# Performance work log

Measured on AMD Instinct MI355X. Metric: run time of the kernel, lower is better.

## Reference

```python
import jax, jax.numpy as jnp
import numpy as np

N_NODES = 40000
N_EDGES = 640000
IN_DIM = 7
HID = 128
N_LAYERS = 5


def setup_inputs() -> dict:
    key = jax.random.key(0)
    ks = jax.random.split(key, 12)
    x = jax.random.normal(ks[0], (N_NODES, IN_DIM), dtype=jnp.float32)
    edge_index = jax.random.randint(ks[1], (2, N_EDGES), 0, N_NODES, dtype=jnp.int64)
    # shift distances away from 0 so 1/d^2 weights stay finite across 5 layers
    dist = jax.random.uniform(ks[2], (N_EDGES,), dtype=jnp.float32) + 0.5
    s_enc = 1.0 / np.sqrt(IN_DIM)
    s_hid = 1.0 / np.sqrt(HID)
    enc_W = jax.random.normal(ks[3], (HID, IN_DIM), dtype=jnp.float32) * s_enc
    enc_b = jax.random.normal(ks[4], (HID,), dtype=jnp.float32) * 0.01
    conv_W = jax.random.normal(ks[5], (N_LAYERS, HID, HID), dtype=jnp.float32) * s_hid * 0.2
    conv_b = jax.random.normal(ks[6], (N_LAYERS, HID), dtype=jnp.float32) * 0.01
    cluster_W = jax.random.normal(ks[7], (3, HID), dtype=jnp.float32) * s_hid
    cluster_b = jax.random.normal(ks[8], (3,), dtype=jnp.float32) * 0.01
    energy_W = jax.random.normal(ks[9], (1, HID), dtype=jnp.float32) * s_hid
    energy_b = jax.random.normal(ks[10], (1,), dtype=jnp.float32) * 0.01
    return {"x": x, "edge_index": edge_index, "dist": dist,
            "enc_W": enc_W, "enc_b": enc_b,
            "conv_W": conv_W, "conv_b": conv_b,
            "cluster_W": cluster_W, "cluster_b": cluster_b,
            "energy_W": energy_W, "energy_b": energy_b}


def reference(x, edge_index, dist, enc_W, enc_b, conv_W, conv_b,
              cluster_W, cluster_b, energy_W, energy_b):
    n = x.shape[0]
    src = edge_index[0]  # x_j: source nodes (PyG source_to_target flow)
    dst = edge_index[1]  # aggregation target
    w = 1.0 / jnp.square(dist + 1e-6)  # [E]
    h = x @ enc_W.T + enc_b  # [N, H]
    for l in range(conv_W.shape[0]):
        # gather -> linear -> inverse-square weight -> scatter-add
        msg = (h[src] @ conv_W[l].T + conv_b[l]) * w[:, None]  # [E, H]
        h = jax.nn.relu(jax.ops.segment_sum(msg, dst, num_segments=n))
    cluster_probs = jax.nn.softmax(h @ cluster_W.T + cluster_b, axis=-1)  # [N, 3]
    energy = h.mean(axis=0, keepdims=True) @ energy_W.T + energy_b  # [1, 1]
    stable = energy < -1.0
    return cluster_probs, energy, stable
```

## Files before the change

kernel.cpp:

```cpp
#include <hip/hip_runtime.h>
#include <hip/hip_fp16.h>

#define NN 40000
#define NE 640000
#define HID 128
#define NL 5
#define NBLK 157

typedef __attribute__((ext_vector_type(8))) short bf16x8;
typedef __attribute__((ext_vector_type(4))) float f32x4;

static __device__ __forceinline__ unsigned short f32_to_bf16_rne(float f) {
  unsigned int u = __float_as_uint(f);
  unsigned int lsb = (u >> 16) & 1u;
  u += 0x7fffu + lsb;
  return (unsigned short)(u >> 16);
}
static __device__ __forceinline__ float bf16_to_f32(unsigned short s) {
  return __uint_as_float(((unsigned int)s) << 16);
}

__global__ void encoder_wconv_kernel(const float* __restrict__ x, const float* __restrict__ encW,
                                     const float* __restrict__ encb, __half* __restrict__ h,
                                     const float* __restrict__ convW,
                                     unsigned short* __restrict__ whi,
                                     unsigned short* __restrict__ wlo) {
  int b = blockIdx.x;
  if (b < 20000) {
    int gid = b * 256 + threadIdx.x;
    int n = gid >> 7, k = gid & 127;
    const float* xp = x + n * 7;
    const float* wp = encW + k * 7;
    float acc = encb[k];
#pragma unroll
    for (int i = 0; i < 7; ++i) acc += xp[i] * wp[i];
    h[gid] = __float2half(acc);
  } else {
    int i = (b - 20000) * 256 + threadIdx.x;
    if (i < NL * HID * HID) {
      float w = convW[i];
      unsigned short hi = f32_to_bf16_rne(w);
      unsigned short lo = f32_to_bf16_rne(w - bf16_to_f32(hi));
      whi[i] = hi;
      wlo[i] = lo;
    }
  }
}

__global__ void hist_kernel(const int* __restrict__ dst, int* __restrict__ cnt,
                            int* __restrict__ rank) {
  int e = blockIdx.x * blockDim.x + threadIdx.x;
  if (e < NE) rank[e] = atomicAdd(&cnt[dst[e]], 1);
}

__global__ void partial_kernel(const int* __restrict__ cnt, int* __restrict__ blocksum) {
  __shared__ int red[4];
  int t = threadIdx.x;
  int idx = blockIdx.x * 256 + t;
  int v = idx < NN ? cnt[idx] : 0;
#pragma unroll
  for (int off = 32; off > 0; off >>= 1) v += __shfl_xor(v, off, 64);
  if ((t & 63) == 0) red[t >> 6] = v;
  __syncthreads();
  if (t == 0) blocksum[blockIdx.x] = red[0] + red[1] + red[2] + red[3];
}

__global__ void scan_small_kernel(const int* __restrict__ blocksum, int* __restrict__ blockoff,
                                  int* __restrict__ row_ptr) {
  __shared__ int sh[256];
  int t = threadIdx.x;
  int v = t < NBLK ? blocksum[t] : 0;
  sh[t] = v;
  __syncthreads();
  for (int off = 1; off < 256; off <<= 1) {
    int u = (t >= off) ? sh[t - off] : 0;
    __syncthreads();
    sh[t] += u;
    __syncthreads();
  }
  if (t < NBLK) blockoff[t] = sh[t] - v;
  if (t == 255) row_ptr[NN] = sh[255];
}

__global__ void rowptr_kernel(const int* __restrict__ cnt, const int* __restrict__ blockoff,
                              int* __restrict__ row_ptr) {
  __shared__ int sh[256];
  int t = threadIdx.x;
  int idx = blockIdx.x * 256 + t;
  int v = idx < NN ? cnt[idx] : 0;
  sh[t] = v;
  __syncthreads();
  for (int off = 1; off < 256; off <<= 1) {
    int u = (t >= off) ? sh[t - off] : 0;
    __syncthreads();
    sh[t] += u;
    __syncthreads();
  }
  if (idx < NN) row_ptr[idx] = blockoff[blockIdx.x] + sh[t] - v;
}

__global__ void scatter_kernel(const int* __restrict__ src, const int* __restrict__ dst,
                               const float* __restrict__ dist,
                               const int* __restrict__ row_ptr, const int* __restrict__ rank,
                               int2* __restrict__ csr_ew) {
  int e = blockIdx.x * blockDim.x + threadIdx.x;
  if (e >= NE) return;
  int pos = row_ptr[dst[e]] + rank[e];
  float dd = dist[e] + 1e-6f;
  float w = 1.0f / (dd * dd);
  csr_ew[pos] = make_int2(src[e], (int)__float_as_uint(w));
}

__global__ void wsum_kernel(const int* __restrict__ row_ptr, const int2* __restrict__ csr_ew,
                            float* __restrict__ wsum) {
  int n = blockIdx.x * blockDim.x + threadIdx.x;
  if (n >= NN) return;
  int s = row_ptr[n], e = row_ptr[n + 1];
  float acc = 0.f;
  for (int i = s; i < e; ++i) acc += __uint_as_float((unsigned)csr_ew[i].y);
  wsum[n] = acc;
}

__global__ void aggregate_kernel(const __half* __restrict__ h, const int* __restrict__ row_ptr,
                                 const int2* __restrict__ csr_ew,
                                 unsigned short* __restrict__ aggh,
                                 unsigned short* __restrict__ aggl) {
  int wid = (blockIdx.x * blockDim.x + threadIdx.x) >> 6;
  int lane = threadIdx.x & 63;
  if (wid >= NN) return;
  int s = __builtin_amdgcn_readfirstlane(row_ptr[wid]);
  int e = __builtin_amdgcn_readfirstlane(row_ptr[wid + 1]);
  int g = lane >> 4;
  int k = lane & 15;
  const __half* hp = h + k * 8;
  float a[8] = {0.f, 0.f, 0.f, 0.f, 0.f, 0.f, 0.f, 0.f};
  int i = s;
  for (; i + 16 <= e; i += 16) {
    uint4 hv[4];
    float wv[4];
#pragma unroll
    for (int u = 0; u < 4; ++u) {
      int2 p = csr_ew[i + u * 4 + g];
      wv[u] = __uint_as_float((unsigned)p.y);
      hv[u] = *reinterpret_cast<const uint4*>(hp + (size_t)p.x * HID);
    }
#pragma unroll
    for (int u = 0; u < 4; ++u) {
      const __half2* q = reinterpret_cast<const __half2*>(&hv[u]);
#pragma unroll
      for (int c = 0; c < 4; ++c) {
        float2 f = __half22float2(q[c]);
        a[2 * c] += wv[u] * f.x;
        a[2 * c + 1] += wv[u] * f.y;
      }
    }
  }
  for (; i < e; i += 4) {
    int j = i + g;
    int jc = j < e ? j : e - 1;
    int2 p = csr_ew[jc];
    float w = (j < e) ? __uint_as_float((unsigned)p.y) : 0.f;
    uint4 hv = *reinterpret_cast<const uint4*>(hp + (size_t)p.x * HID);
    const __half2* q = reinterpret_cast<const __half2*>(&hv);
#pragma unroll
    for (int c = 0; c < 4; ++c) {
      float2 f = __half22float2(q[c]);
      a[2 * c] += w * f.x;
      a[2 * c + 1] += w * f.y;
    }
  }
#pragma unroll
  for (int c = 0; c < 8; ++c) {
    a[c] += __shfl_xor(a[c], 16, 64);
    a[c] += __shfl_xor(a[c], 32, 64);
  }
  if (g == 0) {
    unsigned short hh[8], ll[8];
#pragma unroll
    for (int c = 0; c < 8; ++c) {
      hh[c] = f32_to_bf16_rne(a[c]);
      ll[c] = f32_to_bf16_rne(a[c] - bf16_to_f32(hh[c]));
    }
    *reinterpret_cast<uint4*>(aggh + wid * HID + k * 8) = *reinterpret_cast<const uint4*>(hh);
    *reinterpret_cast<uint4*>(aggl + wid * HID + k * 8) = *reinterpret_cast<const uint4*>(ll);
  }
}

__global__ void __launch_bounds__(256) mfma_linear_kernel(
    const unsigned short* __restrict__ aggh, const unsigned short* __restrict__ aggl,
    const unsigned short* __restrict__ whi, const unsigned short* __restrict__ wlo,
    const float* __restrict__ wsum, const float* __restrict__ b, __half* __restrict__ h) {
  int wave = threadIdx.x >> 6;
  int lane = threadIdx.x & 63;
  int node0 = blockIdx.x * 64 + wave * 16;
  int mrow = lane & 15;
  int kc = (lane >> 4) * 8;

  const unsigned short* pah = aggh + (node0 + mrow) * HID;
  const unsigned short* pal = aggl + (node0 + mrow) * HID;

  f32x4 acc[8];
#pragma unroll
  for (int t = 0; t < 8; ++t) acc[t] = (f32x4){0.f, 0.f, 0.f, 0.f};

#pragma unroll
  for (int s = 0; s < 4; ++s) {
    int joff = s * 32 + kc;
    bf16x8 ah = *reinterpret_cast<const bf16x8*>(pah + joff);
    bf16x8 al = *reinterpret_cast<const bf16x8*>(pal + joff);
#pragma unroll
    for (int t = 0; t < 8; ++t) {
      bf16x8 bh = *reinterpret_cast<const bf16x8*>(whi + (t * 16 + mrow) * HID + joff);
      bf16x8 bl = *reinterpret_cast<const bf16x8*>(wlo + (t * 16 + mrow) * HID + joff);
      acc[t] = __builtin_amdgcn_mfma_f32_16x16x32_bf16(ah, bh, acc[t], 0, 0, 0);
      acc[t] = __builtin_amdgcn_mfma_f32_16x16x32_bf16(ah, bl, acc[t], 0, 0, 0);
      acc[t] = __builtin_amdgcn_mfma_f32_16x16x32_bf16(al, bh, acc[t], 0, 0, 0);
    }
  }

  int nodeBase = node0 + (lane >> 4) * 4;
  float ws4[4];
#pragma unroll
  for (int r = 0; r < 4; ++r) ws4[r] = wsum[nodeBase + r];
#pragma unroll
  for (int t = 0; t < 8; ++t) {
    int kout = t * 16 + mrow;
    float bk = b[kout];
#pragma unroll
    for (int r = 0; r < 4; ++r) {
      float v = acc[t][r] + bk * ws4[r];
      h[(nodeBase + r) * HID + kout] = __float2half(fmaxf(v, 0.f));
    }
  }
}

__global__ void cluster_kernel(const __half* __restrict__ h, const float* __restrict__ cW,
                               const float* __restrict__ cb, float* __restrict__ out) {
  int wid = (blockIdx.x * blockDim.x + threadIdx.x) >> 6;
  int lane = threadIdx.x & 63;
  if (wid >= NN) return;
  float h0 = __half2float(h[wid * HID + lane]);
  float h1 = __half2float(h[wid * HID + 64 + lane]);
  float logit[3];
#pragma unroll
  for (int c = 0; c < 3; ++c) {
    float p = h0 * cW[c * HID + lane] + h1 * cW[c * HID + 64 + lane];
#pragma unroll
    for (int off = 32; off > 0; off >>= 1) p += __shfl_xor(p, off, 64);
    logit[c] = p + cb[c];
  }
  if (lane == 0) {
    float m = fmaxf(logit[0], fmaxf(logit[1], logit[2]));
    float e0 = expf(logit[0] - m), e1 = expf(logit[1] - m), e2 = expf(logit[2] - m);
    float inv = 1.0f / (e0 + e1 + e2);
    out[wid * 3 + 0] = e0 * inv;
    out[wid * 3 + 1] = e1 * inv;
    out[wid * 3 + 2] = e2 * inv;
  }
}

__global__ void colsum_part_kernel(const __half* __restrict__ h, float* __restrict__ partial) {
  int t = threadIdx.x;
  int col = t & 127;
  int lane_id = blockIdx.x * 2 + (t >> 7);
  float acc = 0.f;
  for (int r = lane_id; r < NN; r += 2048) acc += __half2float(h[r * HID + col]);
  partial[lane_id * HID + col] = acc;
}

__global__ void energy_final_kernel(const float* __restrict__ partial,
                                    const float* __restrict__ eW, const float* __restrict__ eb,
                                    float* __restrict__ out) {
  __shared__ float sh[8][HID];
  __shared__ float red[2];
  int t = threadIdx.x;
  int col = t & 127;
  int slot = t >> 7;
  float acc = 0.f;
  for (int i = 0; i < 256; ++i) acc += partial[(slot + 8 * i) * HID + col];
  sh[slot][col] = acc;
  __syncthreads();
  if (t < 128) {
    float s = 0.f;
#pragma unroll
    for (int j = 0; j < 8; ++j) s += sh[j][t];
    float v = s * (1.0f / NN) * eW[t];
#pragma unroll
    for (int off = 32; off > 0; off >>= 1) v += __shfl_xor(v, off, 64);
    if ((t & 63) == 0) red[t >> 6] = v;
  }
  __syncthreads();
  if (t == 0) {
    float e = red[0] + red[1] + eb[0];
    out[NN * 3] = e;
    out[NN * 3 + 1] = (e < -1.0f) ? 1.0f : 0.0f;
  }
}

extern "C" void kernel_launch(void* const* d_in, const int* in_sizes, int n_in,
                              void* d_out, int out_size, void* d_ws, size_t ws_size,
                              hipStream_t stream) {
  const float* x    = (const float*)d_in[0];
  const int*   ei   = (const int*)d_in[1];
  const float* dist = (const float*)d_in[2];
  const float* encW = (const float*)d_in[3];
  const float* encb = (const float*)d_in[4];
  const float* convW = (const float*)d_in[5];
  const float* convb = (const float*)d_in[6];
  const float* cW   = (const float*)d_in[7];
  const float* cb   = (const float*)d_in[8];
  const float* eW   = (const float*)d_in[9];
  const float* eb   = (const float*)d_in[10];
  float* out = (float*)d_out;

  char* ws = (char*)d_ws;
  __half*         h       = (__half*)        (ws + 0);
  unsigned short* aggh    = (unsigned short*)(ws + 10240000);
  unsigned short* aggl    = (unsigned short*)(ws + 20480000);
  int2*           csr_ew  = (int2*)          (ws + 30720000);
  int*            row_ptr = (int*)           (ws + 35840000);
  int*            cnt     = (int*)           (ws + 36000064);
  float*          wsum    = (float*)         (ws + 36160064);
  unsigned short* whi5    = (unsigned short*)(ws + 36320064);
  unsigned short* wlo5    = (unsigned short*)(ws + 36483904);
  int*            rank    = (int*)           (ws + 36647744);
  if (ws_size < (size_t)39207744) return;

  int*   blocksum = (int*)aggh;
  int*   blockoff = (int*)aggh + 512;
  float* partial  = (float*)aggh;

  const int* srcI = ei;
  const int* dstI = ei + NE;

  hipMemsetAsync(cnt, 0, 160000, stream);

  encoder_wconv_kernel<<<20320, 256, 0, stream>>>(x, encW, encb, h, convW, whi5, wlo5);

  hist_kernel<<<(NE + 255) / 256, 256, 0, stream>>>(dstI, cnt, rank);
  partial_kernel<<<NBLK, 256, 0, stream>>>(cnt, blocksum);
  scan_small_kernel<<<1, 256, 0, stream>>>(blocksum, blockoff, row_ptr);
  rowptr_kernel<<<NBLK, 256, 0, stream>>>(cnt, blockoff, row_ptr);
  scatter_kernel<<<(NE + 255) / 256, 256, 0, stream>>>(srcI, dstI, dist, row_ptr, rank, csr_ew);
  wsum_kernel<<<(NN + 255) / 256, 256, 0, stream>>>(row_ptr, csr_ew, wsum);

  for (int l = 0; l < NL; ++l) {
    aggregate_kernel<<<(NN * 64 + 255) / 256, 256, 0, stream>>>(h, row_ptr, csr_ew, aggh, aggl);
    mfma_linear_kernel<<<NN / 64, 256, 0, stream>>>(aggh, aggl,
                                                    whi5 + (size_t)l * HID * HID,
                                                    wlo5 + (size_t)l * HID * HID,
                                                    wsum, convb + (size_t)l * HID, h);
  }

  cluster_kernel<<<(NN * 64 + 255) / 256, 256, 0, stream>>>(h, cW, cb, out);
  colsum_part_kernel<<<1024, 256, 0, stream>>>(h, partial);
  energy_final_kernel<<<1, 1024, 0, stream>>>(partial, eW, eb, out);
}
```

Before: 381.6 us.

## Fuse neighbor aggregation and MFMA linear into one per-layer kernel via LDS

Merges the per-layer aggregate and MFMA linear kernels into one kernel. Each 1024-thread block aggregates 16 nodes (one wave per node) into LDS as bf16 hi/lo splits, then 8 waves each compute one 16-column output tile with MFMA. The hi/lo global round-trip and one launch per layer go away, and h is ping-ponged between two buffers to avoid read/write races. In exchange, half the waves sit idle during the MFMA phase, weights are reloaded per 16-node block, and the large blocks with a barrier may reduce latency hiding for the gather.

```diff
diff --git a/kernel.cpp b/kernel.cpp
--- a/kernel.cpp
+++ b/kernel.cpp
@@ -6,6 +6,7 @@
 #define HID 128
 #define NL 5
 #define NBLK 157
+#define LSTRIDE 136
 
 typedef __attribute__((ext_vector_type(8))) short bf16x8;
 typedef __attribute__((ext_vector_type(4))) float f32x4;
@@ -121,116 +122,103 @@
   wsum[n] = acc;
 }
 
-__global__ void aggregate_kernel(const __half* __restrict__ h, const int* __restrict__ row_ptr,
-                                 const int2* __restrict__ csr_ew,
-                                 unsigned short* __restrict__ aggh,
-                                 unsigned short* __restrict__ aggl) {
-  int wid = (blockIdx.x * blockDim.x + threadIdx.x) >> 6;
+__global__ void __launch_bounds__(1024) fused_layer_kernel(
+    const __half* __restrict__ hin, const int* __restrict__ row_ptr,
+    const int2* __restrict__ csr_ew,
+    const unsigned short* __restrict__ whi, const unsigned short* __restrict__ wlo,
+    const float* __restrict__ wsum, const float* __restrict__ b,
+    __half* __restrict__ hout) {
+  __shared__ __align__(16) unsigned short sAh[16][LSTRIDE];
+  __shared__ __align__(16) unsigned short sAl[16][LSTRIDE];
+  int wave = threadIdx.x >> 6;
   int lane = threadIdx.x & 63;
-  if (wid >= NN) return;
-  int s = __builtin_amdgcn_readfirstlane(row_ptr[wid]);
-  int e = __builtin_amdgcn_readfirstlane(row_ptr[wid + 1]);
-  int g = lane >> 4;
-  int k = lane & 15;
-  const __half* hp = h + k * 8;
-  float a[8] = {0.f, 0.f, 0.f, 0.f, 0.f, 0.f, 0.f, 0.f};
-  int i = s;
-  for (; i + 16 <= e; i += 16) {
-    uint4 hv[4];
-    float wv[4];
-#pragma unroll
-    for (int u = 0; u < 4; ++u) {
-      int2 p = csr_ew[i + u * 4 + g];
-      wv[u] = __uint_as_float((unsigned)p.y);
-      hv[u] = *reinterpret_cast<const uint4*>(hp + (size_t)p.x * HID);
-    }
-#pragma unroll
-    for (int u = 0; u < 4; ++u) {
-      const __half2* q = reinterpret_cast<const __half2*>(&hv[u]);
+  int wid = blockIdx.x * 16 + wave;
+
+  {
+    int s = __builtin_amdgcn_readfirstlane(row_ptr[wid]);
+    int e = __builtin_amdgcn_readfirstlane(row_ptr[wid + 1]);
+    int g = lane >> 4;
+    int k = lane & 15;
+    const __half* hp = hin + k * 8;
+    float a[8] = {0.f, 0.f, 0.f, 0.f, 0.f, 0.f, 0.f, 0.f};
+    int i = s;
+    for (; i + 16 <= e; i += 16) {
+      uint4 hv[4];
+      float wv[4];
+#pragma unroll
+      for (int u = 0; u < 4; ++u) {
+        int2 p = csr_ew[i + u * 4 + g];
+        wv[u] = __uint_as_float((unsigned)p.y);
+        hv[u] = *reinterpret_cast<const uint4*>(hp + (size_t)p.x * HID);
+      }
+#pragma unroll
+      for (int u = 0; u < 4; ++u) {
+        const __half2* q = reinterpret_cast<const __half2*>(&hv[u]);
+#pragma unroll
+        for (int c = 0; c < 4; ++c) {
+          float2 f = __half22float2(q[c]);
+          a[2 * c] += wv[u] * f.x;
+          a[2 * c + 1] += wv[u] * f.y;
+        }
+      }
+    }
+    for (; i < e; i += 4) {
+      int j = i + g;
+      int jc = j < e ? j : e - 1;
+      int2 p = csr_ew[jc];
+      float w = (j < e) ? __uint_as_float((unsigned)p.y) : 0.f;
+      uint4 hv = *reinterpret_cast<const uint4*>(hp + (size_t)p.x * HID);
+      const __half2* q = reinterpret_cast<const __half2*>(&hv);
 #pragma unroll
       for (int c = 0; c < 4; ++c) {
         float2 f = __half22float2(q[c]);
-        a[2 * c] += wv[u] * f.x;
-        a[2 * c + 1] += wv[u] * f.y;
+        a[2 * c] += w * f.x;
+        a[2 * c + 1] += w * f.y;
       }
     }
-  }
-  for (; i < e; i += 4) {
-    int j = i + g;
-    int jc = j < e ? j : e - 1;
-    int2 p = csr_ew[jc];
-    float w = (j < e) ? __uint_as_float((unsigned)p.y) : 0.f;
-    uint4 hv = *reinterpret_cast<const uint4*>(hp + (size_t)p.x * HID);
-    const __half2* q = reinterpret_cast<const __half2*>(&hv);
-#pragma unroll
-    for (int c = 0; c < 4; ++c) {
-      float2 f = __half22float2(q[c]);
-      a[2 * c] += w * f.x;
-      a[2 * c + 1] += w * f.y;
-    }
-  }
-#pragma unroll
-  for (int c = 0; c < 8; ++c) {
-    a[c] += __shfl_xor(a[c], 16, 64);
-    a[c] += __shfl_xor(a[c], 32, 64);
-  }
-  if (g == 0) {
-    unsigned short hh[8], ll[8];
 #pragma unroll
     for (int c = 0; c < 8; ++c) {
-      hh[c] = f32_to_bf16_rne(a[c]);
-      ll[c] = f32_to_bf16_rne(a[c] - bf16_to_f32(hh[c]));
-    }
-    *reinterpret_cast<uint4*>(aggh + wid * HID + k * 8) = *reinterpret_cast<const uint4*>(hh);
-    *reinterpret_cast<uint4*>(aggl + wid * HID + k * 8) = *reinterpret_cast<const uint4*>(ll);
-  }
-}
-
-__global__ void __launch_bounds__(256) mfma_linear_kernel(
-    const unsigned short* __restrict__ aggh, const unsigned short* __restrict__ aggl,
-    const unsigned short* __restrict__ whi, const unsigned short* __restrict__ wlo,
-    const float* __restrict__ wsum, const float* __restrict__ b, __half* __restrict__ h) {
-  int wave = threadIdx.x >> 6;
-  int lane = threadIdx.x & 63;
-  int node0 = blockIdx.x * 64 + wave * 16;
+      a[c] += __shfl_xor(a[c], 16, 64);
+      a[c] += __shfl_xor(a[c], 32, 64);
+    }
+    if (g == 0) {
+      unsigned short hh[8], ll[8];
+#pragma unroll
+      for (int c = 0; c < 8; ++c) {
+        hh[c] = f32_to_bf16_rne(a[c]);
+        ll[c] = f32_to_bf16_rne(a[c] - bf16_to_f32(hh[c]));
+      }
+      *reinterpret_cast<uint4*>(&sAh[wave][k * 8]) = *reinterpret_cast<const uint4*>(hh);
+      *reinterpret_cast<uint4*>(&sAl[wave][k * 8]) = *reinterpret_cast<const uint4*>(ll);
+    }
+  }
+  __syncthreads();
+
+  if (wave >= 8) return;
+  int t = wave;
   int mrow = lane & 15;
   int kc = (lane >> 4) * 8;
 
-  const unsigned short* pah = aggh + (node0 + mrow) * HID;
-  const unsigned short* pal = aggl + (node0 + mrow) * HID;
-
-  f32x4 acc[8];
-#pragma unroll
-  for (int t = 0; t < 8; ++t) acc[t] = (f32x4){0.f, 0.f, 0.f, 0.f};
-
-#pragma unroll
-  for (int s = 0; s < 4; ++s) {
-    int joff = s * 32 + kc;
-    bf16x8 ah = *reinterpret_cast<const bf16x8*>(pah + joff);
-    bf16x8 al = *reinterpret_cast<const bf16x8*>(pal + joff);
-#pragma unroll
-    for (int t = 0; t < 8; ++t) {
-      bf16x8 bh = *reinterpret_cast<const bf16x8*>(whi + (t * 16 + mrow) * HID + joff);
-      bf16x8 bl = *reinterpret_cast<const bf16x8*>(wlo + (t * 16 + mrow) * HID + joff);
-      acc[t] = __builtin_amdgcn_mfma_f32_16x16x32_bf16(ah, bh, acc[t], 0, 0, 0);
-      acc[t] = __builtin_amdgcn_mfma_f32_16x16x32_bf16(ah, bl, acc[t], 0, 0, 0);
-      acc[t] = __builtin_amdgcn_mfma_f32_16x16x32_bf16(al, bh, acc[t], 0, 0, 0);
-    }
-  }
-
-  int nodeBase = node0 + (lane >> 4) * 4;
-  float ws4[4];
-#pragma unroll
-  for (int r = 0; r < 4; ++r) ws4[r] = wsum[nodeBase + r];
-#pragma unroll
-  for (int t = 0; t < 8; ++t) {
-    int kout = t * 16 + mrow;
-    float bk = b[kout];
-#pragma unroll
-    for (int r = 0; r < 4; ++r) {
-      float v = acc[t][r] + bk * ws4[r];
-      h[(nodeBase + r) * HID + kout] = __float2half(fmaxf(v, 0.f));
-    }
+  f32x4 acc = (f32x4){0.f, 0.f, 0.f, 0.f};
+#pragma unroll
+  for (int si = 0; si < 4; ++si) {
+    int joff = si * 32 + kc;
+    bf16x8 ah = *reinterpret_cast<const bf16x8*>(&sAh[mrow][joff]);
+    bf16x8 al = *reinterpret_cast<const bf16x8*>(&sAl[mrow][joff]);
+    bf16x8 bh = *reinterpret_cast<const bf16x8*>(whi + (t * 16 + mrow) * HID + joff);
+    bf16x8 bl = *reinterpret_cast<const bf16x8*>(wlo + (t * 16 + mrow) * HID + joff);
+    acc = __builtin_amdgcn_mfma_f32_16x16x32_bf16(ah, bh, acc, 0, 0, 0);
+    acc = __builtin_amdgcn_mfma_f32_16x16x32_bf16(ah, bl, acc, 0, 0, 0);
+    acc = __builtin_amdgcn_mfma_f32_16x16x32_bf16(al, bh, acc, 0, 0, 0);
+  }
+
+  int nodeBase = blockIdx.x * 16 + (lane >> 4) * 4;
+  int kout = t * 16 + mrow;
+  float bk = b[kout];
+#pragma unroll
+  for (int r = 0; r < 4; ++r) {
+    float v = acc[r] + bk * wsum[nodeBase + r];
+    hout[(nodeBase + r) * HID + kout] = __float2half(fmaxf(v, 0.f));
   }
 }
 
@@ -314,9 +302,9 @@
   float* out = (float*)d_out;
 
   char* ws = (char*)d_ws;
-  __half*         h       = (__half*)        (ws + 0);
-  unsigned short* aggh    = (unsigned short*)(ws + 10240000);
-  unsigned short* aggl    = (unsigned short*)(ws + 20480000);
+  __half*         h1      = (__half*)        (ws + 0);
+  __half*         h2      = (__half*)        (ws + 10240000);
+  char*           scratch = (char*)          (ws + 20480000);
   int2*           csr_ew  = (int2*)          (ws + 30720000);
   int*            row_ptr = (int*)           (ws + 35840000);
   int*            cnt     = (int*)           (ws + 36000064);
@@ -326,16 +314,16 @@
   int*            rank    = (int*)           (ws + 36647744);
   if (ws_size < (size_t)39207744) return;
 
-  int*   blocksum = (int*)aggh;
-  int*   blockoff = (int*)aggh + 512;
-  float* partial  = (float*)aggh;
+  int*   blocksum = (int*)scratch;
+  int*   blockoff = (int*)scratch + 512;
+  float* partial  = (float*)scratch;
 
   const int* srcI = ei;
   const int* dstI = ei + NE;
 
   hipMemsetAsync(cnt, 0, 160000, stream);
 
-  encoder_wconv_kernel<<<20320, 256, 0, stream>>>(x, encW, encb, h, convW, whi5, wlo5);
+  encoder_wconv_kernel<<<20320, 256, 0, stream>>>(x, encW, encb, h1, convW, whi5, wlo5);
 
   hist_kernel<<<(NE + 255) / 256, 256, 0, stream>>>(dstI, cnt, rank);
   partial_kernel<<<NBLK, 256, 0, stream>>>(cnt, blocksum);
@@ -344,15 +332,17 @@
   scatter_kernel<<<(NE + 255) / 256, 256, 0, stream>>>(srcI, dstI, dist, row_ptr, rank, csr_ew);
   wsum_kernel<<<(NN + 255) / 256, 256, 0, stream>>>(row_ptr, csr_ew, wsum);
 
+  __half* hin = h1;
+  __half* hout = h2;
   for (int l = 0; l < NL; ++l) {
-    aggregate_kernel<<<(NN * 64 + 255) / 256, 256, 0, stream>>>(h, row_ptr, csr_ew, aggh, aggl);
-    mfma_linear_kernel<<<NN / 64, 256, 0, stream>>>(aggh, aggl,
-                                                    whi5 + (size_t)l * HID * HID,
-                                                    wlo5 + (size_t)l * HID * HID,
-                                                    wsum, convb + (size_t)l * HID, h);
-  }
-
-  cluster_kernel<<<(NN * 64 + 255) / 256, 256, 0, stream>>>(h, cW, cb, out);
-  colsum_part_kernel<<<1024, 256, 0, stream>>>(h, partial);
+    fused_layer_kernel<<<NN / 16, 1024, 0, stream>>>(hin, row_ptr, csr_ew,
+                                                     whi5 + (size_t)l * HID * HID,
+                                                     wlo5 + (size_t)l * HID * HID,
+                                                     wsum, convb + (size_t)l * HID, hout);
+    __half* tmp = hin; hin = hout; hout = tmp;
+  }
+
+  cluster_kernel<<<(NN * 64 + 255) / 256, 256, 0, stream>>>(hin, cW, cb, out);
+  colsum_part_kernel<<<1024, 256, 0, stream>>>(hin, partial);
   energy_final_kernel<<<1, 1024, 0, stream>>>(partial, eW, eb, out);
 }
```

Measured after the change: 331.1 us. -13.2%, faster.
